# Kernel tuning notes

Hardware: AMD Instinct MI355X
Metric: run time of the kernel (lower is better)

Reference implementation:

```python
import jax, jax.numpy as jnp
import numpy as np

N_HEADS = 32
N_KV_HEADS = 8
HEAD_DIM = 128
DIM = 4096
WINDOW = 4096
BATCH = 32
START_POS = 4095


def setup_inputs() -> dict:
    key = jax.random.key(0)
    ks = jax.random.split(key, 6)
    s = 0.02
    return {
        "x": jax.random.normal(ks[0], (1, 1, BATCH, DIM), jnp.float32),
        "wqkv": jax.random.normal(ks[1], (DIM, (N_HEADS + 2 * N_KV_HEADS) * HEAD_DIM), jnp.float32) * s,
        "wo": jax.random.normal(ks[2], (DIM, DIM), jnp.float32) * s,
        "rot_mat": jax.random.normal(ks[3], (HEAD_DIM, HEAD_DIM), jnp.float32) * s,
        "cache_k": jax.random.normal(ks[4], (N_KV_HEADS, BATCH, WINDOW, HEAD_DIM), jnp.float32),
        "cache_v": jax.random.normal(ks[5], (N_KV_HEADS, BATCH, WINDOW, HEAD_DIM), jnp.float32),
        "start_pos": START_POS,
    }


def reference(x, wqkv, wo, rot_mat, cache_k, cache_v, start_pos):
    B = x.shape[2]
    D = HEAD_DIM
    group = N_HEADS // N_KV_HEADS  # 4 q heads per kv head (GQA)

    # fused QKV projection for the single decode token: [B, (nq+2*nkv)*D]
    xqkv = jnp.einsum('bh,hf->bf', x[0, 0], wqkv)
    q = xqkv[:, : N_HEADS * D].reshape(B, N_HEADS, D)
    k = xqkv[:, N_HEADS * D: (N_HEADS + N_KV_HEADS) * D].reshape(B, N_KV_HEADS, D)
    v = xqkv[:, (N_HEADS + N_KV_HEADS) * D:].reshape(B, N_KV_HEADS, D)

    # rotary embedding applied as a matmul by a [D, D] rotation matrix
    q = jnp.einsum('bnd,de->bne', q, rot_mat) * (D ** -0.5)
    k = jnp.einsum('bnd,de->bne', k, rot_mat)

    # sliding-window KV cache update at current_pos (cache: [nkv, B, W, D])
    current_pos = start_pos % WINDOW
    cache_k = cache_k.at[:, :, current_pos, :].set(jnp.transpose(k, (1, 0, 2)))
    cache_v = cache_v.at[:, :, current_pos, :].set(jnp.transpose(v, (1, 0, 2)))

    layer_slice = min(start_pos + 1, WINDOW)  # static python int
    keys = cache_k[:, :, :layer_slice]    # [nkv, B, S, D]
    values = cache_v[:, :, :layer_slice]  # [nkv, B, S, D]

    qg = q.reshape(B, N_KV_HEADS, group, D)
    scores = jnp.einsum('bkgd,kbsd->bkgs', qg, keys)       # [B, nkv, g, S]
    attn = jax.nn.softmax(scores, axis=-1)
    out = jnp.einsum('bkgs,kbsd->bkgd', attn, values)      # [B, nkv, g, D]
    out = out.reshape(B, N_HEADS * D)

    dense = out @ wo  # wo pre-transposed: [H, H], output features last
    return dense.reshape(1, 1, B, DIM)
```

## Files before the change

### kernel.cpp

```cpp
#include <hip/hip_runtime.h>
#include <math.h>

#define B 32
#define NH 32
#define NKV 8
#define GRP 4
#define HD 128
#define DIM 4096
#define NQKV 6144
#define WIN 4096
#define KS 32
#define SPLIT 8
#define SCHUNK (WIN / SPLIT)

__global__ __launch_bounds__(256)
void gemv32_partial(const float* __restrict__ X, const float* __restrict__ W,
                    float* __restrict__ part, int K, int N) {
  const int f  = blockIdx.x * 256 + threadIdx.x;
  const int kc = blockIdx.y;
  const int kchunk = K / KS;
  const int k0 = kc * kchunk;

  __shared__ float xs[128][36];

  float acc[B];
#pragma unroll
  for (int b = 0; b < B; ++b) acc[b] = 0.f;

  for (int kb = 0; kb < kchunk; kb += 128) {
    __syncthreads();
    for (int idx = threadIdx.x; idx < B * 128; idx += 256) {
      int bb = idx >> 7;
      int kk = idx & 127;
      xs[kk][bb] = X[(size_t)bb * K + (k0 + kb + kk)];
    }
    __syncthreads();

    const float* wp = W + (size_t)(k0 + kb) * N + f;
#pragma unroll 4
    for (int kk = 0; kk < 128; ++kk) {
      float w = wp[(size_t)kk * N];
      const float4* xr = (const float4*)&xs[kk][0];
#pragma unroll
      for (int b4 = 0; b4 < 8; ++b4) {
        float4 xv = xr[b4];
        acc[b4 * 4 + 0] += xv.x * w;
        acc[b4 * 4 + 1] += xv.y * w;
        acc[b4 * 4 + 2] += xv.z * w;
        acc[b4 * 4 + 3] += xv.w * w;
      }
    }
  }

  float* pp = part + (size_t)kc * B * N + f;
#pragma unroll
  for (int b = 0; b < B; ++b) pp[(size_t)b * N] = acc[b];
}

__global__ __launch_bounds__(256)
void reduce_partials(const float* __restrict__ part, float* __restrict__ out,
                     int total) {
  int idx = blockIdx.x * 256 + threadIdx.x;
  if (idx >= total) return;
  float s = 0.f;
#pragma unroll
  for (int kc = 0; kc < KS; ++kc) s += part[(size_t)kc * total + idx];
  out[idx] = s;
}

__global__ __launch_bounds__(128)
void rotary_kernel(const float* __restrict__ xqkv, const float* __restrict__ rot,
                   float* __restrict__ qrot, float* __restrict__ krot) {
  const int b = blockIdx.x;
  const int h = blockIdx.y;
  const int e = threadIdx.x;

  __shared__ float vec[HD];
  vec[e] = xqkv[(size_t)b * NQKV + h * HD + e];
  __syncthreads();

  float s = 0.f;
#pragma unroll 8
  for (int d = 0; d < HD; ++d) s += vec[d] * rot[d * HD + e];

  const float QSCALE = 0.08838834764831845f * 1.4426950408889634f;
  if (h < NH) {
    qrot[((size_t)b * NH + h) * HD + e] = s * QSCALE;
  } else {
    krot[((size_t)b * NKV + (h - NH)) * HD + e] = s;
  }
}

__global__ __launch_bounds__(256)
void attn_partial(const float* __restrict__ cache_k, const float* __restrict__ cache_v,
                  const float* __restrict__ qrot, const float* __restrict__ krot,
                  const float* __restrict__ xqkv, const int* __restrict__ start_pos,
                  float* __restrict__ o_part, float* __restrict__ l_part) {
  const int pair = blockIdx.x;
  const int b    = pair >> 3;
  const int kvh  = pair & 7;
  const int chunk = blockIdx.y;

  const int sp    = start_pos[0];
  const int cur   = sp & (WIN - 1);
  const int slice = (sp + 1 < WIN) ? (sp + 1) : WIN;

  const int tid  = threadIdx.x;
  const int wave = tid >> 6;
  const int lane = tid & 63;
  const int half = lane >> 5;
  const int l32  = lane & 31;
  const int hw   = wave * 2 + half;

  float4 q[GRP];
#pragma unroll
  for (int g = 0; g < GRP; ++g)
    q[g] = *(const float4*)(qrot + ((size_t)(b * NH + kvh * GRP + g)) * HD + l32 * 4);

  const float4* kbase = (const float4*)(cache_k + ((size_t)(kvh * B + b)) * WIN * HD);
  const float4* vbase = (const float4*)(cache_v + ((size_t)(kvh * B + b)) * WIN * HD);

  float  l[GRP] = {0.f, 0.f, 0.f, 0.f};
  float4 acc[GRP] = {};

  const int s0 = chunk * SCHUNK;
  int rem = slice - s0 - hw;
  int n_i = rem <= 0 ? 0 : ((rem + 7) >> 3);
  if (n_i > SCHUNK / 8) n_i = SCHUNK / 8;

#pragma unroll 2
  for (int i = 0; i < n_i; ++i) {
    const int p = s0 + i * 8 + hw;
    float4 k4 = kbase[(size_t)p * 32 + l32];
    float4 v4 = vbase[(size_t)p * 32 + l32];

    float s[GRP];
#pragma unroll
    for (int g = 0; g < GRP; ++g)
      s[g] = q[g].x * k4.x + q[g].y * k4.y + q[g].z * k4.z + q[g].w * k4.w;

#pragma unroll
    for (int off = 16; off > 0; off >>= 1) {
#pragma unroll
      for (int g = 0; g < GRP; ++g) s[g] += __shfl_xor(s[g], off);
    }

#pragma unroll
    for (int g = 0; g < GRP; ++g) {
      float w = exp2f(s[g]);
      l[g] += w;
      acc[g].x += w * v4.x; acc[g].y += w * v4.y;
      acc[g].z += w * v4.z; acc[g].w += w * v4.w;
    }
  }

  if (chunk == (cur >> 9) && hw == (cur & 7)) {
    float4 kst = kbase[(size_t)cur * 32 + l32];
    float4 vst = vbase[(size_t)cur * 32 + l32];
    const float4 knew = *(const float4*)(krot + ((size_t)(b * NKV + kvh)) * HD + l32 * 4);
    const float4 vnew = *(const float4*)(xqkv + (size_t)b * NQKV + (NH + NKV + kvh) * HD + l32 * 4);
    float sst[GRP], snw[GRP];
#pragma unroll
    for (int g = 0; g < GRP; ++g) {
      sst[g] = q[g].x * kst.x + q[g].y * kst.y + q[g].z * kst.z + q[g].w * kst.w;
      snw[g] = q[g].x * knew.x + q[g].y * knew.y + q[g].z * knew.z + q[g].w * knew.w;
    }
#pragma unroll
    for (int off = 16; off > 0; off >>= 1) {
#pragma unroll
      for (int g = 0; g < GRP; ++g) {
        sst[g] += __shfl_xor(sst[g], off);
        snw[g] += __shfl_xor(snw[g], off);
      }
    }
#pragma unroll
    for (int g = 0; g < GRP; ++g) {
      float wst = exp2f(sst[g]);
      float wnw = exp2f(snw[g]);
      l[g] += wnw - wst;
      acc[g].x += wnw * vnew.x - wst * vst.x;
      acc[g].y += wnw * vnew.y - wst * vst.y;
      acc[g].z += wnw * vnew.z - wst * vst.z;
      acc[g].w += wnw * vnew.w - wst * vst.w;
    }
  }

#pragma unroll
  for (int g = 0; g < GRP; ++g) {
    l[g] += __shfl_xor(l[g], 32);
    acc[g].x += __shfl_xor(acc[g].x, 32);
    acc[g].y += __shfl_xor(acc[g].y, 32);
    acc[g].z += __shfl_xor(acc[g].z, 32);
    acc[g].w += __shfl_xor(acc[g].w, 32);
  }

  __shared__ float red_l[4][GRP];
  __shared__ float red_o[4][GRP][HD];
  if (lane == 0) {
#pragma unroll
    for (int g = 0; g < GRP; ++g) red_l[wave][g] = l[g];
  }
  if (half == 0) {
#pragma unroll
    for (int g = 0; g < GRP; ++g)
      *(float4*)&red_o[wave][g][l32 * 4] = acc[g];
  }
  __syncthreads();

  const size_t pc = (size_t)pair * SPLIT + chunk;
  for (int idx = tid; idx < GRP * HD; idx += 256) {
    int g = idx >> 7, d = idx & 127;
    float o = red_o[0][g][d] + red_o[1][g][d] + red_o[2][g][d] + red_o[3][g][d];
    o_part[(pc * GRP + g) * HD + d] = o;
  }
  if (tid < GRP) {
    l_part[pc * GRP + tid] =
        red_l[0][tid] + red_l[1][tid] + red_l[2][tid] + red_l[3][tid];
  }
}

__global__ __launch_bounds__(128)
void attn_combine(const float* __restrict__ o_part, const float* __restrict__ l_part,
                  float* __restrict__ attn_out) {
  const int bid = blockIdx.x;
  const int b = bid >> 5, n = bid & 31;
  const int pair = b * NKV + (n >> 2);
  const int g = n & 3;
  const int d = threadIdx.x;

  float lsum = 0.f, osum = 0.f;
#pragma unroll
  for (int c = 0; c < SPLIT; ++c) {
    size_t pc = (size_t)pair * SPLIT + c;
    lsum += l_part[pc * GRP + g];
    osum += o_part[(pc * GRP + g) * HD + d];
  }
  attn_out[(size_t)b * DIM + n * HD + d] = osum / lsum;
}

extern "C" void kernel_launch(void* const* d_in, const int* in_sizes, int n_in,
                              void* d_out, int out_size, void* d_ws, size_t ws_size,
                              hipStream_t stream) {
  (void)in_sizes; (void)n_in; (void)out_size; (void)ws_size;

  const float* x    = (const float*)d_in[0];
  const float* wqkv = (const float*)d_in[1];
  const float* wo   = (const float*)d_in[2];
  const float* rot  = (const float*)d_in[3];
  const float* ck   = (const float*)d_in[4];
  const float* cv   = (const float*)d_in[5];
  const int*   sp   = (const int*)d_in[6];
  float* out = (float*)d_out;

  float* ws       = (float*)d_ws;
  float* part     = ws;
  float* xqkv     = part + (size_t)KS * B * NQKV;
  float* qrot     = xqkv + (size_t)B * NQKV;
  float* krot     = qrot + (size_t)B * NH * HD;
  float* o_part   = krot + (size_t)B * NKV * HD;
  float* l_part   = o_part + (size_t)B * NKV * SPLIT * GRP * HD;
  float* attn_out = l_part + (size_t)B * NKV * SPLIT * GRP;

  gemv32_partial<<<dim3(NQKV / 256, KS), 256, 0, stream>>>(x, wqkv, part, DIM, NQKV);
  reduce_partials<<<(B * NQKV) / 256, 256, 0, stream>>>(part, xqkv, B * NQKV);

  rotary_kernel<<<dim3(B, NH + NKV), 128, 0, stream>>>(xqkv, rot, qrot, krot);

  attn_partial<<<dim3(B * NKV, SPLIT), 256, 0, stream>>>(ck, cv, qrot, krot, xqkv,
                                                         sp, o_part, l_part);
  attn_combine<<<B * NH, 128, 0, stream>>>(o_part, l_part, attn_out);

  gemv32_partial<<<dim3(DIM / 256, KS), 256, 0, stream>>>(attn_out, wo, part, DIM, DIM);
  reduce_partials<<<(B * DIM) / 256, 256, 0, stream>>>(part, out, B * DIM);
}
```

Before: 326.1 us.

## Compute two GEMV outputs per thread and remap attention lanes per query head

```diff
diff --git a/kernel.cpp b/kernel.cpp
--- a/kernel.cpp
+++ b/kernel.cpp
@@ -13,23 +13,31 @@
 #define SPLIT 8
 #define SCHUNK (WIN / SPLIT)
 
-__global__ __launch_bounds__(256)
+__device__ __forceinline__ float fast_exp2(float x) {
+#if __has_builtin(__builtin_amdgcn_exp2f)
+  return __builtin_amdgcn_exp2f(x);
+#else
+  return exp2f(x);
+#endif
+}
+
+__global__ __launch_bounds__(128)
 void gemv32_partial(const float* __restrict__ X, const float* __restrict__ W,
                     float* __restrict__ part, int K, int N) {
-  const int f  = blockIdx.x * 256 + threadIdx.x;
+  const int f  = (blockIdx.x * 128 + threadIdx.x) * 2;
   const int kc = blockIdx.y;
   const int kchunk = K / KS;
   const int k0 = kc * kchunk;
 
   __shared__ float xs[128][36];
 
-  float acc[B];
-#pragma unroll
-  for (int b = 0; b < B; ++b) acc[b] = 0.f;
+  float acc0[B], acc1[B];
+#pragma unroll
+  for (int b = 0; b < B; ++b) { acc0[b] = 0.f; acc1[b] = 0.f; }
 
   for (int kb = 0; kb < kchunk; kb += 128) {
     __syncthreads();
-    for (int idx = threadIdx.x; idx < B * 128; idx += 256) {
+    for (int idx = threadIdx.x; idx < B * 128; idx += 128) {
       int bb = idx >> 7;
       int kk = idx & 127;
       xs[kk][bb] = X[(size_t)bb * K + (k0 + kb + kk)];
@@ -37,24 +45,27 @@
     __syncthreads();
 
     const float* wp = W + (size_t)(k0 + kb) * N + f;
-#pragma unroll 4
+#pragma unroll 8
     for (int kk = 0; kk < 128; ++kk) {
-      float w = wp[(size_t)kk * N];
+      float2 w2 = *(const float2*)(wp + (size_t)kk * N);
       const float4* xr = (const float4*)&xs[kk][0];
 #pragma unroll
       for (int b4 = 0; b4 < 8; ++b4) {
         float4 xv = xr[b4];
-        acc[b4 * 4 + 0] += xv.x * w;
-        acc[b4 * 4 + 1] += xv.y * w;
-        acc[b4 * 4 + 2] += xv.z * w;
-        acc[b4 * 4 + 3] += xv.w * w;
+        acc0[b4 * 4 + 0] += xv.x * w2.x;  acc1[b4 * 4 + 0] += xv.x * w2.y;
+        acc0[b4 * 4 + 1] += xv.y * w2.x;  acc1[b4 * 4 + 1] += xv.y * w2.y;
+        acc0[b4 * 4 + 2] += xv.z * w2.x;  acc1[b4 * 4 + 2] += xv.z * w2.y;
+        acc0[b4 * 4 + 3] += xv.w * w2.x;  acc1[b4 * 4 + 3] += xv.w * w2.y;
       }
     }
   }
 
   float* pp = part + (size_t)kc * B * N + f;
 #pragma unroll
-  for (int b = 0; b < B; ++b) pp[(size_t)b * N] = acc[b];
+  for (int b = 0; b < B; ++b) {
+    float2 o; o.x = acc0[b]; o.y = acc1[b];
+    *(float2*)(pp + (size_t)b * N) = o;
+  }
 }
 
 __global__ __launch_bounds__(256)
@@ -110,18 +121,22 @@
   const int lane = tid & 63;
   const int half = lane >> 5;
   const int l32  = lane & 31;
+  const int g    = l32 >> 3;
+  const int dc   = l32 & 7;
   const int hw   = wave * 2 + half;
 
-  float4 q[GRP];
-#pragma unroll
-  for (int g = 0; g < GRP; ++g)
-    q[g] = *(const float4*)(qrot + ((size_t)(b * NH + kvh * GRP + g)) * HD + l32 * 4);
+  float4 q[4];
+  {
+    const float* qp = qrot + ((size_t)(b * NH + kvh * GRP + g)) * HD + dc * 4;
+#pragma unroll
+    for (int j = 0; j < 4; ++j) q[j] = *(const float4*)(qp + j * 32);
+  }
 
   const float4* kbase = (const float4*)(cache_k + ((size_t)(kvh * B + b)) * WIN * HD);
   const float4* vbase = (const float4*)(cache_v + ((size_t)(kvh * B + b)) * WIN * HD);
 
-  float  l[GRP] = {0.f, 0.f, 0.f, 0.f};
-  float4 acc[GRP] = {};
+  float  l = 0.f;
+  float4 acc[4] = {};
 
   const int s0 = chunk * SCHUNK;
   int rem = slice - s0 - hw;
@@ -131,87 +146,82 @@
 #pragma unroll 2
   for (int i = 0; i < n_i; ++i) {
     const int p = s0 + i * 8 + hw;
-    float4 k4 = kbase[(size_t)p * 32 + l32];
-    float4 v4 = vbase[(size_t)p * 32 + l32];
-
-    float s[GRP];
-#pragma unroll
-    for (int g = 0; g < GRP; ++g)
-      s[g] = q[g].x * k4.x + q[g].y * k4.y + q[g].z * k4.z + q[g].w * k4.w;
-
-#pragma unroll
-    for (int off = 16; off > 0; off >>= 1) {
-#pragma unroll
-      for (int g = 0; g < GRP; ++g) s[g] += __shfl_xor(s[g], off);
-    }
-
-#pragma unroll
-    for (int g = 0; g < GRP; ++g) {
-      float w = exp2f(s[g]);
-      l[g] += w;
-      acc[g].x += w * v4.x; acc[g].y += w * v4.y;
-      acc[g].z += w * v4.z; acc[g].w += w * v4.w;
-    }
+    const size_t rb = (size_t)p * 32 + dc;
+    float4 k0 = kbase[rb + 0],  k1 = kbase[rb + 8],
+           k2 = kbase[rb + 16], k3 = kbase[rb + 24];
+    float4 v0 = vbase[rb + 0],  v1 = vbase[rb + 8],
+           v2 = vbase[rb + 16], v3 = vbase[rb + 24];
+
+    float s = q[0].x * k0.x + q[0].y * k0.y + q[0].z * k0.z + q[0].w * k0.w
+            + q[1].x * k1.x + q[1].y * k1.y + q[1].z * k1.z + q[1].w * k1.w
+            + q[2].x * k2.x + q[2].y * k2.y + q[2].z * k2.z + q[2].w * k2.w
+            + q[3].x * k3.x + q[3].y * k3.y + q[3].z * k3.z + q[3].w * k3.w;
+
+    s += __shfl_xor(s, 1);
+    s += __shfl_xor(s, 2);
+    s += __shfl_xor(s, 4);
+
+    float w = fast_exp2(s);
+    l += w;
+    acc[0].x += w * v0.x; acc[0].y += w * v0.y; acc[0].z += w * v0.z; acc[0].w += w * v0.w;
+    acc[1].x += w * v1.x; acc[1].y += w * v1.y; acc[1].z += w * v1.z; acc[1].w += w * v1.w;
+    acc[2].x += w * v2.x; acc[2].y += w * v2.y; acc[2].z += w * v2.z; acc[2].w += w * v2.w;
+    acc[3].x += w * v3.x; acc[3].y += w * v3.y; acc[3].z += w * v3.z; acc[3].w += w * v3.w;
   }
 
   if (chunk == (cur >> 9) && hw == (cur & 7)) {
-    float4 kst = kbase[(size_t)cur * 32 + l32];
-    float4 vst = vbase[(size_t)cur * 32 + l32];
-    const float4 knew = *(const float4*)(krot + ((size_t)(b * NKV + kvh)) * HD + l32 * 4);
-    const float4 vnew = *(const float4*)(xqkv + (size_t)b * NQKV + (NH + NKV + kvh) * HD + l32 * 4);
-    float sst[GRP], snw[GRP];
-#pragma unroll
-    for (int g = 0; g < GRP; ++g) {
-      sst[g] = q[g].x * kst.x + q[g].y * kst.y + q[g].z * kst.z + q[g].w * kst.w;
-      snw[g] = q[g].x * knew.x + q[g].y * knew.y + q[g].z * knew.z + q[g].w * knew.w;
-    }
-#pragma unroll
-    for (int off = 16; off > 0; off >>= 1) {
-#pragma unroll
-      for (int g = 0; g < GRP; ++g) {
-        sst[g] += __shfl_xor(sst[g], off);
-        snw[g] += __shfl_xor(snw[g], off);
-      }
-    }
-#pragma unroll
-    for (int g = 0; g < GRP; ++g) {
-      float wst = exp2f(sst[g]);
-      float wnw = exp2f(snw[g]);
-      l[g] += wnw - wst;
-      acc[g].x += wnw * vnew.x - wst * vst.x;
-      acc[g].y += wnw * vnew.y - wst * vst.y;
-      acc[g].z += wnw * vnew.z - wst * vst.z;
-      acc[g].w += wnw * vnew.w - wst * vst.w;
-    }
-  }
-
-#pragma unroll
-  for (int g = 0; g < GRP; ++g) {
-    l[g] += __shfl_xor(l[g], 32);
-    acc[g].x += __shfl_xor(acc[g].x, 32);
-    acc[g].y += __shfl_xor(acc[g].y, 32);
-    acc[g].z += __shfl_xor(acc[g].z, 32);
-    acc[g].w += __shfl_xor(acc[g].w, 32);
+    const size_t rb = (size_t)cur * 32 + dc;
+    const float* kp = krot + ((size_t)(b * NKV + kvh)) * HD + dc * 4;
+    const float* vp = xqkv + (size_t)b * NQKV + (NH + NKV + kvh) * HD + dc * 4;
+    float sst = 0.f, snw = 0.f;
+    float4 kst[4], vst[4], knw[4], vnw[4];
+#pragma unroll
+    for (int j = 0; j < 4; ++j) {
+      kst[j] = kbase[rb + j * 8];
+      vst[j] = vbase[rb + j * 8];
+      knw[j] = *(const float4*)(kp + j * 32);
+      vnw[j] = *(const float4*)(vp + j * 32);
+      sst += q[j].x * kst[j].x + q[j].y * kst[j].y + q[j].z * kst[j].z + q[j].w * kst[j].w;
+      snw += q[j].x * knw[j].x + q[j].y * knw[j].y + q[j].z * knw[j].z + q[j].w * knw[j].w;
+    }
+    sst += __shfl_xor(sst, 1); sst += __shfl_xor(sst, 2); sst += __shfl_xor(sst, 4);
+    snw += __shfl_xor(snw, 1); snw += __shfl_xor(snw, 2); snw += __shfl_xor(snw, 4);
+    float wst = fast_exp2(sst);
+    float wnw = fast_exp2(snw);
+    l += wnw - wst;
+#pragma unroll
+    for (int j = 0; j < 4; ++j) {
+      acc[j].x += wnw * vnw[j].x - wst * vst[j].x;
+      acc[j].y += wnw * vnw[j].y - wst * vst[j].y;
+      acc[j].z += wnw * vnw[j].z - wst * vst[j].z;
+      acc[j].w += wnw * vnw[j].w - wst * vst[j].w;
+    }
+  }
+
+  l += __shfl_xor(l, 32);
+#pragma unroll
+  for (int j = 0; j < 4; ++j) {
+    acc[j].x += __shfl_xor(acc[j].x, 32);
+    acc[j].y += __shfl_xor(acc[j].y, 32);
+    acc[j].z += __shfl_xor(acc[j].z, 32);
+    acc[j].w += __shfl_xor(acc[j].w, 32);
   }
 
   __shared__ float red_l[4][GRP];
   __shared__ float red_o[4][GRP][HD];
-  if (lane == 0) {
-#pragma unroll
-    for (int g = 0; g < GRP; ++g) red_l[wave][g] = l[g];
-  }
   if (half == 0) {
 #pragma unroll
-    for (int g = 0; g < GRP; ++g)
-      *(float4*)&red_o[wave][g][l32 * 4] = acc[g];
+    for (int j = 0; j < 4; ++j)
+      *(float4*)&red_o[wave][g][j * 32 + dc * 4] = acc[j];
+    if (dc == 0) red_l[wave][g] = l;
   }
   __syncthreads();
 
   const size_t pc = (size_t)pair * SPLIT + chunk;
   for (int idx = tid; idx < GRP * HD; idx += 256) {
-    int g = idx >> 7, d = idx & 127;
-    float o = red_o[0][g][d] + red_o[1][g][d] + red_o[2][g][d] + red_o[3][g][d];
-    o_part[(pc * GRP + g) * HD + d] = o;
+    int gg = idx >> 7, d = idx & 127;
+    float o = red_o[0][gg][d] + red_o[1][gg][d] + red_o[2][gg][d] + red_o[3][gg][d];
+    o_part[(pc * GRP + gg) * HD + d] = o;
   }
   if (tid < GRP) {
     l_part[pc * GRP + tid] =
@@ -261,7 +271,7 @@
   float* l_part   = o_part + (size_t)B * NKV * SPLIT * GRP * HD;
   float* attn_out = l_part + (size_t)B * NKV * SPLIT * GRP;
 
-  gemv32_partial<<<dim3(NQKV / 256, KS), 256, 0, stream>>>(x, wqkv, part, DIM, NQKV);
+  gemv32_partial<<<dim3(NQKV / 256, KS), 128, 0, stream>>>(x, wqkv, part, DIM, NQKV);
   reduce_partials<<<(B * NQKV) / 256, 256, 0, stream>>>(part, xqkv, B * NQKV);
 
   rotary_kernel<<<dim3(B, NH + NKV), 128, 0, stream>>>(xqkv, rot, qrot, krot);
@@ -270,6 +280,6 @@
                                                          sp, o_part, l_part);
   attn_combine<<<B * NH, 128, 0, stream>>>(o_part, l_part, attn_out);
 
-  gemv32_partial<<<dim3(DIM / 256, KS), 256, 0, stream>>>(attn_out, wo, part, DIM, DIM);
+  gemv32_partial<<<dim3(DIM / 256, KS), 128, 0, stream>>>(attn_out, wo, part, DIM, DIM);
   reduce_partials<<<(B * DIM) / 256, 256, 0, stream>>>(part, out, B * DIM);
 }
```

After: 456.2 us. +39.9%, slower.

## Double SPLIT for attention, prefetch next KV row, use hardware exp2

Applied to the files above, without the earlier changes.

```diff
diff --git a/kernel.cpp b/kernel.cpp
--- a/kernel.cpp
+++ b/kernel.cpp
@@ -10,8 +10,16 @@
 #define NQKV 6144
 #define WIN 4096
 #define KS 32
-#define SPLIT 8
+#define SPLIT 16
 #define SCHUNK (WIN / SPLIT)
+
+__device__ __forceinline__ float fast_exp2(float x) {
+#if __has_builtin(__builtin_amdgcn_exp2f)
+  return __builtin_amdgcn_exp2f(x);
+#else
+  return exp2f(x);
+#endif
+}
 
 __global__ __launch_bounds__(256)
 void gemv32_partial(const float* __restrict__ X, const float* __restrict__ W,
@@ -128,33 +136,41 @@
   int n_i = rem <= 0 ? 0 : ((rem + 7) >> 3);
   if (n_i > SCHUNK / 8) n_i = SCHUNK / 8;
 
-#pragma unroll 2
-  for (int i = 0; i < n_i; ++i) {
-    const int p = s0 + i * 8 + hw;
-    float4 k4 = kbase[(size_t)p * 32 + l32];
-    float4 v4 = vbase[(size_t)p * 32 + l32];
-
+  auto body = [&](float4 k4, float4 v4) {
     float s[GRP];
 #pragma unroll
     for (int g = 0; g < GRP; ++g)
       s[g] = q[g].x * k4.x + q[g].y * k4.y + q[g].z * k4.z + q[g].w * k4.w;
-
 #pragma unroll
     for (int off = 16; off > 0; off >>= 1) {
 #pragma unroll
       for (int g = 0; g < GRP; ++g) s[g] += __shfl_xor(s[g], off);
     }
-
 #pragma unroll
     for (int g = 0; g < GRP; ++g) {
-      float w = exp2f(s[g]);
+      float w = fast_exp2(s[g]);
       l[g] += w;
       acc[g].x += w * v4.x; acc[g].y += w * v4.y;
       acc[g].z += w * v4.z; acc[g].w += w * v4.w;
     }
-  }
-
-  if (chunk == (cur >> 9) && hw == (cur & 7)) {
+  };
+
+  if (n_i > 0) {
+    size_t rb = ((size_t)(s0 + hw)) * 32 + l32;
+    float4 k4 = kbase[rb];
+    float4 v4 = vbase[rb];
+#pragma unroll 2
+    for (int i = 1; i < n_i; ++i) {
+      rb += 8 * 32;
+      float4 kn = kbase[rb];
+      float4 vn = vbase[rb];
+      body(k4, v4);
+      k4 = kn; v4 = vn;
+    }
+    body(k4, v4);
+  }
+
+  if (chunk == (cur >> 8) && hw == (cur & 7)) {
     float4 kst = kbase[(size_t)cur * 32 + l32];
     float4 vst = vbase[(size_t)cur * 32 + l32];
     const float4 knew = *(const float4*)(krot + ((size_t)(b * NKV + kvh)) * HD + l32 * 4);
@@ -175,8 +191,8 @@
     }
 #pragma unroll
     for (int g = 0; g < GRP; ++g) {
-      float wst = exp2f(sst[g]);
-      float wnw = exp2f(snw[g]);
+      float wst = fast_exp2(sst[g]);
+      float wnw = fast_exp2(snw[g]);
       l[g] += wnw - wst;
       acc[g].x += wnw * vnew.x - wst * vst.x;
       acc[g].y += wnw * vnew.y - wst * vst.y;
@@ -254,11 +270,11 @@
 
   float* ws       = (float*)d_ws;
   float* part     = ws;
+  float* o_part   = ws;
   float* xqkv     = part + (size_t)KS * B * NQKV;
   float* qrot     = xqkv + (size_t)B * NQKV;
   float* krot     = qrot + (size_t)B * NH * HD;
-  float* o_part   = krot + (size_t)B * NKV * HD;
-  float* l_part   = o_part + (size_t)B * NKV * SPLIT * GRP * HD;
+  float* l_part   = krot + (size_t)B * NKV * HD;
   float* attn_out = l_part + (size_t)B * NKV * SPLIT * GRP;
 
   gemv32_partial<<<dim3(NQKV / 256, KS), 256, 0, stream>>>(x, wqkv, part, DIM, NQKV);
```

Result: faster. 317.6 us (-2.6%).
